# Performance work log

Hardware: AMD Instinct MI355X
Metric: run time of the kernel (lower is better)

The kernel has to match this reference:

```python
import jax, jax.numpy as jnp
import numpy as np

TAU = 2.0   # spikingjelly LIFNode default tau
VTH = 1.0   # config.vthreshold

@jax.custom_vjp
def atan_spike(x):
    # heaviside forward, ATan surrogate backward (spikingjelly surrogate.ATan, alpha=2)
    return (x >= 0).astype(x.dtype)

def _atan_fwd(x):
    return atan_spike(x), x

def _atan_bwd(x, g):
    alpha = 2.0
    return (g * (alpha / 2.0) / (1.0 + (jnp.pi / 2.0 * alpha * x) ** 2),)

atan_spike.defvjp(_atan_fwd, _atan_bwd)

def layer_norm(x, eps=1e-6):
    m = jnp.mean(x, axis=-1, keepdims=True)
    v = jnp.mean((x - m) ** 2, axis=-1, keepdims=True)
    return (x - m) * jax.lax.rsqrt(v + eps)

def time_shift(x):
    # ZeroPad2d((0,0,1,-1)): xx[:, t] = x[:, t-1], xx[:, 0] = 0
    return jnp.pad(x, ((0, 0), (1, 0), (0, 0)))[:, :-1]

def lif_multistep(x4):
    # spikingjelly LIFNode, step_mode='m', decay_input=True, hard reset to v_reset=0
    def step(v, xt):
        v = v + (xt - v) / TAU
        s = atan_spike(v - VTH)
        return v * (1.0 - s), s
    _, spikes = jax.lax.scan(step, jnp.zeros_like(x4[0]), x4)
    return spikes

def wkv(w, u, k, v):
    # RWKV-v4 numerically-stable WKV scan. w: [C] (negative), u: [C], k,v: [B,T,C]
    B, T, C = k.shape
    def step(carry, kv):
        aa, bb, pp = carry
        kt, vt = kv
        ww = u + kt
        p = jnp.maximum(pp, ww)
        e1 = jnp.exp(pp - p); e2 = jnp.exp(ww - p)
        y = (e1 * aa + e2 * vt) / (e1 * bb + e2)
        ww2 = pp + w
        p2 = jnp.maximum(ww2, kt)
        f1 = jnp.exp(ww2 - p2); f2 = jnp.exp(kt - p2)
        return (f1 * aa + f2 * vt, f1 * bb + f2, p2), y
    init = (jnp.zeros((B, C), k.dtype), jnp.zeros((B, C), k.dtype),
            jnp.full((B, C), -1e38, k.dtype))
    _, ys = jax.lax.scan(step, init, (jnp.moveaxis(k, 1, 0), jnp.moveaxis(v, 1, 0)))
    return jnp.moveaxis(ys, 0, 1)

def time_mix(h, time_decay, time_first, tmk, tmv, tmr, Wk, Wv, Wr, Wo):
    xx = time_shift(h)
    xk = h * tmk + xx * (1 - tmk)
    xv = h * tmv + xx * (1 - tmv)
    xr = h * tmr + xx * (1 - tmr)
    k = jnp.einsum('btc,oc->bto', xk, Wk)
    v = jnp.einsum('btc,oc->bto', xv, Wv)
    sr = jax.nn.sigmoid(jnp.einsum('btc,oc->bto', xr, Wr))
    y = wkv(-jnp.exp(time_decay), time_first, k, v)
    return jnp.einsum('btc,oc->bto', sr * y, Wo)

def channel_mix(h, cmk, cmr, Wck, Wcv, Wcr):
    xx = time_shift(h)
    xk = h * cmk + xx * (1 - cmk)
    xr = h * cmr + xx * (1 - cmr)
    k = jnp.square(jax.nn.relu(jnp.einsum('btc,hc->bth', xk, Wck)))
    kv = jnp.einsum('bth,ch->btc', k, Wcv)
    return jax.nn.sigmoid(jnp.einsum('btc,oc->bto', xr, Wcr)) * kv

def _forward(x, rt, time_decay, time_first, tmix_k, tmix_v, tmix_r,
             Wk, Wv, Wr, Wo, cmix_k, cmix_r, Wck, Wcv, Wcr,
             Wrm, brm, Wam, bam):
    B, P1, C = x.shape
    xc = jnp.concatenate([x, jnp.broadcast_to(rt, (B, P1, C))], axis=1)  # [B, 2*P1, C]
    att = time_mix(layer_norm(xc), time_decay, time_first,
                   tmix_k, tmix_v, tmix_r, Wk, Wv, Wr, Wo)
    att = lif_multistep(jnp.broadcast_to(att, (4,) + att.shape)).mean(0)
    xc = xc + att
    ffn = channel_mix(layer_norm(xc), cmix_k, cmix_r, Wck, Wcv, Wcr)
    ffn = lif_multistep(jnp.broadcast_to(ffn, (4,) + ffn.shape)).mean(0)
    xc = xc + ffn
    xo, rtok = xc[:, :P1], xc[:, P1:]
    r = jnp.einsum('bpc,qc->bpq', rtok, Wrm) + brm   # restruction_token_MLP [B,P1,P1]
    r = jnp.swapaxes(r, 1, 2)                        # permute(0,2,1)
    r = jnp.einsum('bpq,cq->bpc', r, Wam) + bam      # another_MLP [B,P1,C]
    return xo + xo * r

def setup_inputs() -> dict:
    key = jax.random.key(0)
    ks = jax.random.split(key, 20)
    B, P1, C = 8, 256, 1024
    H = 4 * C
    s = 0.02
    f32 = jnp.float32
    return {
        'x': jax.random.normal(ks[0], (B, P1, C), f32),
        'rt': jax.random.normal(ks[1], (1, P1, C), f32) * 0.5,
        'time_decay': jax.random.normal(ks[2], (C,), f32),
        'time_first': jax.random.normal(ks[3], (C,), f32) * 0.3,
        'tmix_k': jax.random.uniform(ks[4], (1, 1, C), f32),
        'tmix_v': jax.random.uniform(ks[5], (1, 1, C), f32),
        'tmix_r': jax.random.uniform(ks[6], (1, 1, C), f32),
        'Wk': jax.random.normal(ks[7], (C, C), f32) * s,
        'Wv': jax.random.normal(ks[8], (C, C), f32) * s,
        'Wr': jax.random.normal(ks[9], (C, C), f32) * s,
        'Wo': jax.random.normal(ks[10], (C, C), f32) * s,
        'cmix_k': jax.random.uniform(ks[11], (1, 1, C), f32),
        'cmix_r': jax.random.uniform(ks[12], (1, 1, C), f32),
        'Wck': jax.random.normal(ks[13], (H, C), f32) * s,
        'Wcv': jax.random.normal(ks[14], (C, H), f32) * s,
        'Wcr': jax.random.normal(ks[15], (C, C), f32) * s,
        'Wrm': jax.random.normal(ks[16], (P1, C), f32) * s,
        'brm': jax.random.normal(ks[17], (P1,), f32) * s,
        'Wam': jax.random.normal(ks[18], (C, P1), f32) * s,
        'bam': jax.random.normal(ks[19], (C,), f32) * s,
    }

def reference(x, rt, time_decay, time_first, tmix_k, tmix_v, tmix_r,
              Wk, Wv, Wr, Wo, cmix_k, cmix_r, Wck, Wcv, Wcr,
              Wrm, brm, Wam, bam):
    return _forward(x, rt, time_decay, time_first, tmix_k, tmix_v, tmix_r,
                    Wk, Wv, Wr, Wo, cmix_k, cmix_r, Wck, Wcv, Wcr,
                    Wrm, brm, Wam, bam)
```

## Files before the change

kernel.cpp:

```cpp
#include <hip/hip_runtime.h>
#include <hip/hip_bf16.h>
#include <math.h>
#include <stdint.h>

#define TB_ 8
#define TT_ 512
#define TC_ 1024
#define WKV_NCH 32
#define WKV_L 16

typedef __attribute__((ext_vector_type(8))) short bf16x8;
typedef __attribute__((ext_vector_type(4))) short s16x4;
typedef __attribute__((ext_vector_type(4))) float f32x4;

__device__ __forceinline__ float b2f(short u) {
  union { unsigned int i; float f; } x;
  x.i = ((unsigned int)(unsigned short)u) << 16;
  return x.f;
}
__device__ __forceinline__ short f2b(float f) {
  __hip_bfloat16 h = __float2bfloat16(f);
  return __builtin_bit_cast(short, h);
}
__device__ __forceinline__ float sigm(float x) { return 1.0f / (1.0f + expf(-x)); }

__device__ __forceinline__ float lif4(float a) {
  float v = 0.0f, acc = 0.0f;
#pragma unroll
  for (int i = 0; i < 4; ++i) {
    v += (a - v) * 0.5f;
    float s = (v >= 1.0f) ? 1.0f : 0.0f;
    acc += s;
    v *= (1.0f - s);
  }
  return acc * 0.25f;
}

__device__ __forceinline__ void gload16(const void* g, void* l) {
  __builtin_amdgcn_global_load_lds(
      (__attribute__((address_space(1))) void*)(g),
      (__attribute__((address_space(3))) void*)(l), 16, 0, 0);
}

template <int N>
__device__ __forceinline__ void waitv() {
  if constexpr (N == 0)  asm volatile("s_waitcnt vmcnt(0)" ::: "memory");
  else if constexpr (N == 2)  asm volatile("s_waitcnt vmcnt(2)" ::: "memory");
  else if constexpr (N == 4)  asm volatile("s_waitcnt vmcnt(4)" ::: "memory");
  else if constexpr (N == 8)  asm volatile("s_waitcnt vmcnt(8)" ::: "memory");
  else if constexpr (N == 12) asm volatile("s_waitcnt vmcnt(12)" ::: "memory");
  else static_assert(N == 0, "unsupported vmcnt");
}
__device__ __forceinline__ void barrier_() {
  asm volatile("s_barrier" ::: "memory");
}


__global__ __launch_bounds__(256) void ln_mix3(
    const float* __restrict__ x, const float* __restrict__ rt,
    const float* __restrict__ tmk, const float* __restrict__ tmv,
    const float* __restrict__ tmr, float* __restrict__ xc,
    short* __restrict__ xk, short* __restrict__ xv, short* __restrict__ xr) {
  __shared__ float red[256];
  int row = blockIdx.x;
  int t = row & 511, b = row >> 9;
  int tid = threadIdx.x;
  const float* src = (t < 256) ? x + (int64_t)(b * 256 + t) * TC_
                               : rt + (int64_t)(t - 256) * TC_;
  float4 v = ((const float4*)src)[tid];
  ((float4*)(xc + (int64_t)row * TC_))[tid] = v;
  red[tid] = v.x + v.y + v.z + v.w;
  __syncthreads();
  for (int off = 128; off > 0; off >>= 1) {
    if (tid < off) red[tid] += red[tid + off];
    __syncthreads();
  }
  float mean = red[0] * (1.0f / 1024.0f);
  __syncthreads();
  float dx = v.x - mean, dy = v.y - mean, dz = v.z - mean, dw = v.w - mean;
  red[tid] = dx * dx + dy * dy + dz * dz + dw * dw;
  __syncthreads();
  for (int off = 128; off > 0; off >>= 1) {
    if (tid < off) red[tid] += red[tid + off];
    __syncthreads();
  }
  float rs = 1.0f / sqrtf(red[0] * (1.0f / 1024.0f) + 1e-6f);
  float c0 = dx * rs, c1 = dy * rs, c2 = dz * rs, c3 = dw * rs;
  float p0 = 0.f, p1 = 0.f, p2 = 0.f, p3 = 0.f;
  if (t > 0) {
    int tp = t - 1;
    const float* srcp = (tp < 256) ? x + (int64_t)(b * 256 + tp) * TC_
                                   : rt + (int64_t)(tp - 256) * TC_;
    __syncthreads();
    float4 w4 = ((const float4*)srcp)[tid];
    red[tid] = w4.x + w4.y + w4.z + w4.w;
    __syncthreads();
    for (int off = 128; off > 0; off >>= 1) {
      if (tid < off) red[tid] += red[tid + off];
      __syncthreads();
    }
    float meanp = red[0] * (1.0f / 1024.0f);
    __syncthreads();
    float ex = w4.x - meanp, ey = w4.y - meanp, ez = w4.z - meanp,
          ew = w4.w - meanp;
    red[tid] = ex * ex + ey * ey + ez * ez + ew * ew;
    __syncthreads();
    for (int off = 128; off > 0; off >>= 1) {
      if (tid < off) red[tid] += red[tid + off];
      __syncthreads();
    }
    float rsp = 1.0f / sqrtf(red[0] * (1.0f / 1024.0f) + 1e-6f);
    p0 = ex * rsp; p1 = ey * rsp; p2 = ez * rsp; p3 = ew * rsp;
  }
  int c = tid * 4;
  int64_t o = (int64_t)row * TC_ + c;
  float m0, m1, m2, m3;
  s16x4 ov;
  m0 = tmk[c]; m1 = tmk[c + 1]; m2 = tmk[c + 2]; m3 = tmk[c + 3];
  ov.x = f2b(c0 * m0 + p0 * (1.0f - m0));
  ov.y = f2b(c1 * m1 + p1 * (1.0f - m1));
  ov.z = f2b(c2 * m2 + p2 * (1.0f - m2));
  ov.w = f2b(c3 * m3 + p3 * (1.0f - m3));
  *(s16x4*)(xk + o) = ov;
  m0 = tmv[c]; m1 = tmv[c + 1]; m2 = tmv[c + 2]; m3 = tmv[c + 3];
  ov.x = f2b(c0 * m0 + p0 * (1.0f - m0));
  ov.y = f2b(c1 * m1 + p1 * (1.0f - m1));
  ov.z = f2b(c2 * m2 + p2 * (1.0f - m2));
  ov.w = f2b(c3 * m3 + p3 * (1.0f - m3));
  *(s16x4*)(xv + o) = ov;
  m0 = tmr[c]; m1 = tmr[c + 1]; m2 = tmr[c + 2]; m3 = tmr[c + 3];
  ov.x = f2b(c0 * m0 + p0 * (1.0f - m0));
  ov.y = f2b(c1 * m1 + p1 * (1.0f - m1));
  ov.z = f2b(c2 * m2 + p2 * (1.0f - m2));
  ov.w = f2b(c3 * m3 + p3 * (1.0f - m3));
  *(s16x4*)(xr + o) = ov;
}

__global__ __launch_bounds__(256) void ln_mix2(const float* __restrict__ xc,
                                               const float* __restrict__ cmk,
                                               const float* __restrict__ cmr,
                                               short* __restrict__ xk,
                                               short* __restrict__ xr) {
  __shared__ float red[256];
  int row = blockIdx.x;
  int t = row & 511;
  int tid = threadIdx.x;
  float4 v = ((const float4*)(xc + (int64_t)row * TC_))[tid];
  red[tid] = v.x + v.y + v.z + v.w;
  __syncthreads();
  for (int off = 128; off > 0; off >>= 1) {
    if (tid < off) red[tid] += red[tid + off];
    __syncthreads();
  }
  float mean = red[0] * (1.0f / 1024.0f);
  __syncthreads();
  float dx = v.x - mean, dy = v.y - mean, dz = v.z - mean, dw = v.w - mean;
  red[tid] = dx * dx + dy * dy + dz * dz + dw * dw;
  __syncthreads();
  for (int off = 128; off > 0; off >>= 1) {
    if (tid < off) red[tid] += red[tid + off];
    __syncthreads();
  }
  float rs = 1.0f / sqrtf(red[0] * (1.0f / 1024.0f) + 1e-6f);
  float c0 = dx * rs, c1 = dy * rs, c2 = dz * rs, c3 = dw * rs;
  float p0 = 0.f, p1 = 0.f, p2 = 0.f, p3 = 0.f;
  if (t > 0) {
    __syncthreads();
    float4 w4 = ((const float4*)(xc + (int64_t)(row - 1) * TC_))[tid];
    red[tid] = w4.x + w4.y + w4.z + w4.w;
    __syncthreads();
    for (int off = 128; off > 0; off >>= 1) {
      if (tid < off) red[tid] += red[tid + off];
      __syncthreads();
    }
    float meanp = red[0] * (1.0f / 1024.0f);
    __syncthreads();
    float ex = w4.x - meanp, ey = w4.y - meanp, ez = w4.z - meanp,
          ew = w4.w - meanp;
    red[tid] = ex * ex + ey * ey + ez * ez + ew * ew;
    __syncthreads();
    for (int off = 128; off > 0; off >>= 1) {
      if (tid < off) red[tid] += red[tid + off];
      __syncthreads();
    }
    float rsp = 1.0f / sqrtf(red[0] * (1.0f / 1024.0f) + 1e-6f);
    p0 = ex * rsp; p1 = ey * rsp; p2 = ez * rsp; p3 = ew * rsp;
  }
  int c = tid * 4;
  float k0 = cmk[c], k1 = cmk[c + 1], k2 = cmk[c + 2], k3 = cmk[c + 3];
  float r0 = cmr[c], r1 = cmr[c + 1], r2 = cmr[c + 2], r3 = cmr[c + 3];
  s16x4 ok, orr;
  ok.x = f2b(c0 * k0 + p0 * (1.0f - k0));
  ok.y = f2b(c1 * k1 + p1 * (1.0f - k1));
  ok.z = f2b(c2 * k2 + p2 * (1.0f - k2));
  ok.w = f2b(c3 * k3 + p3 * (1.0f - k3));
  orr.x = f2b(c0 * r0 + p0 * (1.0f - r0));
  orr.y = f2b(c1 * r1 + p1 * (1.0f - r1));
  orr.z = f2b(c2 * r2 + p2 * (1.0f - r2));
  orr.w = f2b(c3 * r3 + p3 * (1.0f - r3));
  *(s16x4*)(xk + (int64_t)row * TC_ + c) = ok;
  *(s16x4*)(xr + (int64_t)row * TC_ + c) = orr;
}

__global__ __launch_bounds__(256) void cvt_b(const float* __restrict__ src,
                                             short* __restrict__ dst) {
  int64_t i = (int64_t)(blockIdx.x * 256 + threadIdx.x) * 8;
  float4 a = *(const float4*)(src + i);
  float4 b = *(const float4*)(src + i + 4);
  bf16x8 o;
  o[0] = f2b(a.x); o[1] = f2b(a.y); o[2] = f2b(a.z); o[3] = f2b(a.w);
  o[4] = f2b(b.x); o[5] = f2b(b.y); o[6] = f2b(b.z); o[7] = f2b(b.w);
  *(bf16x8*)(dst + i) = o;
}

__global__ __launch_bounds__(256) void cvt_rtok(const float* __restrict__ xc,
                                                short* __restrict__ dst) {
  int i = blockIdx.x * 256 + threadIdx.x;
  int b = i >> 15;
  int rem = i & 32767;
  const float* s = xc + (int64_t)b * 524288 + 262144 + (int64_t)rem * 8;
  float4 a = *(const float4*)s;
  float4 c = *(const float4*)(s + 4);
  bf16x8 o;
  o[0] = f2b(a.x); o[1] = f2b(a.y); o[2] = f2b(a.z); o[3] = f2b(a.w);
  o[4] = f2b(c.x); o[5] = f2b(c.y); o[6] = f2b(c.z); o[7] = f2b(c.w);
  *(bf16x8*)(dst + (int64_t)i * 8) = o;
}

__global__ __launch_bounds__(256) void cvt_all(
    const float* __restrict__ Wk, const float* __restrict__ Wv,
    const float* __restrict__ Wr, const float* __restrict__ Wo,
    const float* __restrict__ Wcr, const float* __restrict__ Wcv,
    const float* __restrict__ Wrm, const float* __restrict__ Wam,
    short* __restrict__ bWk, short* __restrict__ bWv, short* __restrict__ bWr,
    short* __restrict__ bWo, short* __restrict__ bWcr, short* __restrict__ bWcv,
    short* __restrict__ bWrm, short* __restrict__ bWam,
    float* __restrict__ S) {
  int bid = blockIdx.x;
  if (bid >= 4864) {
    int row = (bid - 4864) * 4 + (threadIdx.x >> 6);
    int lane = threadIdx.x & 63;
    float4 v = ((const float4*)(Wam + (int64_t)row * 256))[lane];
    float s = v.x + v.y + v.z + v.w;
    for (int off = 32; off > 0; off >>= 1) s += __shfl_down(s, off);
    if (lane == 0) S[row] = s;
    return;
  }
  const float* src; short* dst; int base;
  if (bid < 512)       { src = Wk;  dst = bWk;  base = bid; }
  else if (bid < 1024) { src = Wv;  dst = bWv;  base = bid - 512; }
  else if (bid < 1536) { src = Wr;  dst = bWr;  base = bid - 1024; }
  else if (bid < 2048) { src = Wo;  dst = bWo;  base = bid - 1536; }
  else if (bid < 2560) { src = Wcr; dst = bWcr; base = bid - 2048; }
  else if (bid < 4608) { src = Wcv; dst = bWcv; base = bid - 2560; }
  else if (bid < 4736) { src = Wrm; dst = bWrm; base = bid - 4608; }
  else                 { src = Wam; dst = bWam; base = bid - 4736; }
  int64_t i = ((int64_t)base * 256 + threadIdx.x) * 8;
  float4 a = *(const float4*)(src + i);
  float4 b = *(const float4*)(src + i + 4);
  bf16x8 o;
  o[0] = f2b(a.x); o[1] = f2b(a.y); o[2] = f2b(a.z); o[3] = f2b(a.w);
  o[4] = f2b(b.x); o[5] = f2b(b.y); o[6] = f2b(b.z); o[7] = f2b(b.w);
  *(bf16x8*)(dst + i) = o;
}

__global__ __launch_bounds__(256) void wkv_p1(const float* __restrict__ td,
                                              const short* __restrict__ K,
                                              const short* __restrict__ V,
                                              float* __restrict__ Ca,
                                              float* __restrict__ Da,
                                              float* __restrict__ Qa) {
  int bx = blockIdx.x;
  int ch = bx >> 5;
  int b = (bx >> 2) & 7;
  int c = (bx & 3) * 256 + threadIdx.x;
  float w = -expf(td[c]);
  float aa = 0.0f, bb = 0.0f, pp = -1e38f;
  int64_t base = ((int64_t)b * TT_ + ch * WKV_L) * TC_ + c;
#pragma unroll
  for (int t = 0; t < WKV_L; ++t) {
    int64_t o = base + (int64_t)t * TC_;
    float kt = b2f(K[o]), vt = b2f(V[o]);
    float ww2 = pp + w;
    float p2 = fmaxf(ww2, kt);
    float e1 = expf(ww2 - p2);
    float e2 = expf(kt - p2);
    aa = e1 * aa + e2 * vt;
    bb = e1 * bb + e2;
    pp = p2;
  }
  int idx = ch * 8192 + b * 1024 + c;
  Ca[idx] = aa; Da[idx] = bb; Qa[idx] = pp;
}

__global__ __launch_bounds__(256) void wkv_p2(const float* __restrict__ td,
                                              const float* __restrict__ Ca,
                                              const float* __restrict__ Da,
                                              const float* __restrict__ Qa,
                                              float* __restrict__ Aa,
                                              float* __restrict__ Ba,
                                              float* __restrict__ Pa) {
  int i = blockIdx.x * 256 + threadIdx.x;
  int c = i & (TC_ - 1);
  float wL = -expf(td[c]) * (float)WKV_L;
  float aa = 0.0f, bb = 0.0f, pp = -1e38f;
#pragma unroll 4
  for (int ch = 0; ch < WKV_NCH; ++ch) {
    int idx = ch * 8192 + i;
    Aa[idx] = aa; Ba[idx] = bb; Pa[idx] = pp;
    float ppw = pp + wL;
    float q = Qa[idx];
    float p2 = fmaxf(ppw, q);
    float ea = expf(ppw - p2);
    float eb = expf(q - p2);
    aa = aa * ea + Ca[idx] * eb;
    bb = bb * ea + Da[idx] * eb;
    pp = p2;
  }
}

__global__ __launch_bounds__(256) void wkv_p3(const float* __restrict__ td,
                                              const float* __restrict__ tf,
                                              const short* __restrict__ K,
                                              const short* __restrict__ V,
                                              const short* __restrict__ SR,
                                              short* __restrict__ SRY,
                                              const float* __restrict__ Aa,
                                              const float* __restrict__ Ba,
                                              const float* __restrict__ Pa) {
  int bx = blockIdx.x;
  int ch = bx >> 5;
  int b = (bx >> 2) & 7;
  int c = (bx & 3) * 256 + threadIdx.x;
  float w = -expf(td[c]);
  float u = tf[c];
  int idx = ch * 8192 + b * 1024 + c;
  float aa = Aa[idx], bb = Ba[idx], pp = Pa[idx];
  int64_t base = ((int64_t)b * TT_ + ch * WKV_L) * TC_ + c;
#pragma unroll
  for (int t = 0; t < WKV_L; ++t) {
    int64_t o = base + (int64_t)t * TC_;
    float kt = b2f(K[o]), vt = b2f(V[o]);
    float ww = u + kt;
    float p = fmaxf(pp, ww);
    float E1 = expf(pp - p);
    float E2 = expf(ww - p);
    float y = (E1 * aa + E2 * vt) / (E1 * bb + E2);
    SRY[o] = f2b(y * b2f(SR[o]));
    float ww2 = pp + w;
    float p2 = fmaxf(ww2, kt);
    float e1 = expf(ww2 - p2);
    float e2 = expf(kt - p2);
    aa = e1 * aa + e2 * vt;
    bb = e1 * bb + e2;
    pp = p2;
  }
}

template <int EPI>
__global__ __launch_bounds__(512, 1) void gemm2p(
    const short* __restrict__ A, const short* __restrict__ B,
    void* __restrict__ Cp, int M, int N, int K, int Kst,
    const float* __restrict__ e0, const float* __restrict__ e1,
    const float* __restrict__ e2, const void* __restrict__ e3) {
  __shared__ short lds[2 * 32768];
  const int tid = threadIdx.x;

  const unsigned gx = gridDim.x, gy = gridDim.y;
  const unsigned nwg = gx * gy;
  const unsigned lin = blockIdx.x + gx * blockIdx.y;
  const unsigned cs = nwg >> 3;
  const unsigned nl = (lin & 7) * cs + (lin >> 3);
  const unsigned bxs = nl % gx;
  const unsigned bys = nl / gx;

  const int brow = bys * 128;
  const int bcol = bxs * 128;

  const int srow = ((tid >> 6) << 4) + (tid & 15);
  const int skc = ((tid >> 4) & 3) * 8;
  const short* gA = A + (int64_t)(brow + srow) * Kst + skc;
  const short* gB = B + (int64_t)(bcol + srow) * Kst + skc;

  const int lane = tid & 63, wid = tid >> 6;
  const int wr = wid >> 2, wc = wid & 3;

  f32x4 acc[4][2] = {};

#define RD_A(rb, kh, m) \
  (*(const bf16x8*)(lds + (rb) * 32768 + (kh) * 8192 + (wr * 4 + (m)) * 512 + lane * 8))
#define RD_B(rb, kh, n) \
  (*(const bf16x8*)(lds + (rb) * 32768 + 16384 + (kh) * 8192 + (wc * 2 + (n)) * 512 + lane * 8))
#define ST_A(sb, kh, kt) \
  gload16(gA + (kt) * 64 + (kh) * 32, lds + (sb) * 32768 + (kh) * 8192 + tid * 8)
#define ST_B(sb, kh, kt) \
  gload16(gB + (kt) * 64 + (kh) * 32, lds + (sb) * 32768 + 16384 + (kh) * 8192 + tid * 8)
#define MM(am, bn, i, j) \
  acc[i][j] = __builtin_amdgcn_mfma_f32_16x16x32_bf16(am, bn, acc[i][j], 0, 0, 0)

  const int nt = K / 64;
  ST_A(0, 0, 0); ST_B(0, 0, 0); ST_A(0, 1, 0); ST_B(0, 1, 0);
  waitv<2>();
  barrier_();

  for (int t = 0; t < nt - 1; ++t) {
    const int rb = t & 1, sb = rb ^ 1, kn = t + 1;
    {
      bf16x8 a0 = RD_A(rb, 0, 0), a1 = RD_A(rb, 0, 1);
      bf16x8 a2 = RD_A(rb, 0, 2), a3 = RD_A(rb, 0, 3);
      bf16x8 b0 = RD_B(rb, 0, 0), b1 = RD_B(rb, 0, 1);
      ST_A(sb, 0, kn); ST_B(sb, 0, kn);
      MM(a0, b0, 0, 0); MM(a0, b1, 0, 1); MM(a1, b0, 1, 0); MM(a1, b1, 1, 1);
      MM(a2, b0, 2, 0); MM(a2, b1, 2, 1); MM(a3, b0, 3, 0); MM(a3, b1, 3, 1);
      waitv<2>();
      barrier_();
    }
    {
      bf16x8 a0 = RD_A(rb, 1, 0), a1 = RD_A(rb, 1, 1);
      bf16x8 a2 = RD_A(rb, 1, 2), a3 = RD_A(rb, 1, 3);
      bf16x8 b0 = RD_B(rb, 1, 0), b1 = RD_B(rb, 1, 1);
      ST_A(sb, 1, kn); ST_B(sb, 1, kn);
      MM(a0, b0, 0, 0); MM(a0, b1, 0, 1); MM(a1, b0, 1, 0); MM(a1, b1, 1, 1);
      MM(a2, b0, 2, 0); MM(a2, b1, 2, 1); MM(a3, b0, 3, 0); MM(a3, b1, 3, 1);
      waitv<2>();
      barrier_();
    }
  }
  {
    waitv<0>();
    barrier_();
    const int rb = (nt - 1) & 1;
#pragma unroll
    for (int kh = 0; kh < 2; ++kh) {
      bf16x8 a0 = RD_A(rb, kh, 0), a1 = RD_A(rb, kh, 1);
      bf16x8 a2 = RD_A(rb, kh, 2), a3 = RD_A(rb, kh, 3);
      bf16x8 b0 = RD_B(rb, kh, 0), b1 = RD_B(rb, kh, 1);
      MM(a0, b0, 0, 0); MM(a0, b1, 0, 1); MM(a1, b0, 1, 0); MM(a1, b1, 1, 1);
      MM(a2, b0, 2, 0); MM(a2, b1, 2, 1); MM(a3, b0, 3, 0); MM(a3, b1, 3, 1);
    }
  }
#undef RD_A
#undef RD_B
#undef ST_A
#undef ST_B
#undef MM

  const int r0 = brow + wr * 64 + (lane >> 4) * 4;
  const int c0 = bcol + wc * 32 + (lane & 15);
#pragma unroll
  for (int m = 0; m < 4; ++m) {
#pragma unroll
    for (int j = 0; j < 4; ++j) {
      int row = r0 + m * 16 + j;
#pragma unroll
      for (int n = 0; n < 2; ++n) {
        int col = c0 + n * 16;
        float v = acc[m][n][j];
        int64_t idx = (int64_t)row * N + col;
        if (EPI == 1) {
          ((short*)Cp)[idx] = f2b(sigm(v));
        } else if (EPI == 4) {
          float* XC = (float*)Cp;
          XC[idx] = XC[idx] + lif4(v);
        } else if (EPI == 5) {
          float* XC = (float*)Cp;
          float srr = b2f(((const short*)e3)[idx]);
          XC[idx] = XC[idx] + lif4(v * srr);
        }
      }
    }
  }
}

template <int EPI>
__global__ __launch_bounds__(512, 1) void gemm256(
    const short* __restrict__ A, const short* __restrict__ B,
    void* __restrict__ Cp, int M, int N, int K, int Kst,
    int64_t sA, int64_t sB, int64_t sC) {
  __shared__ short lds[2 * 32768];
  const int tid = threadIdx.x;

  const unsigned gx = gridDim.x, gy = gridDim.y;
  const unsigned nwg = gx * gy * gridDim.z;
  const unsigned lin = blockIdx.x + gx * (blockIdx.y + gy * blockIdx.z);
  const unsigned cs = nwg >> 3;
  const unsigned nl = (lin & 7) * cs + (lin >> 3);
  const unsigned bxs = nl % gx;
  const unsigned tmp = nl / gx;
  const unsigned bys = tmp % gy;
  const unsigned bz = tmp / gy;

  const int brow = bys * 256;
  const int bcol = bxs * 256;
  const short* Ab = A + bz * sA;
  const short* Bb = B + bz * sB;

  const short* gA[2];
  const short* gB[2];
  int loff[2];
#pragma unroll
  for (int c = 0; c < 2; ++c) {
    int p = c * 512 + tid;
    int u = p >> 6, s = p & 63;
    gA[c] = Ab + (int64_t)(brow + u * 16 + (s & 15)) * Kst + (s >> 4) * 8;
    gB[c] = Bb + (int64_t)(bcol + u * 16 + (s & 15)) * Kst + (s >> 4) * 8;
    loff[c] = p * 8;
  }

  const int lane = tid & 63, wid = tid >> 6;
  const int wr = wid >> 2, wc = wid & 3;

  f32x4 acc[8][4] = {};

#define RD_A(rb, kh, m) \
  (*(const bf16x8*)(lds + (rb) * 32768 + (kh) * 8192 + (wr * 8 + (m)) * 512 + lane * 8))
#define RD_B(rb, kh, n) \
  (*(const bf16x8*)(lds + (rb) * 32768 + 16384 + (kh) * 8192 + (wc * 4 + (n)) * 512 + lane * 8))
#define ST_A(sb, kh, kt)                                                     \
  {                                                                          \
    gload16(gA[0] + (kt) * 64 + (kh) * 32,                                   \
            lds + (sb) * 32768 + (kh) * 8192 + loff[0]);                     \
    gload16(gA[1] + (kt) * 64 + (kh) * 32,                                   \
            lds + (sb) * 32768 + (kh) * 8192 + loff[1]);                     \
  }
#define ST_B(sb, kh, kt)                                                     \
  {                                                                          \
    gload16(gB[0] + (kt) * 64 + (kh) * 32,                                   \
            lds + (sb) * 32768 + 16384 + (kh) * 8192 + loff[0]);             \
    gload16(gB[1] + (kt) * 64 + (kh) * 32,                                   \
            lds + (sb) * 32768 + 16384 + (kh) * 8192 + loff[1]);             \
  }
#define MM(am, bn, i, j) \
  acc[i][j] = __builtin_amdgcn_mfma_f32_16x16x32_bf16(am, bn, acc[i][j], 0, 0, 0)

  const int nt = K / 64;
  ST_A(0, 0, 0); ST_B(0, 0, 0); ST_A(0, 1, 0); ST_B(0, 1, 0);
  waitv<4>();
  barrier_();

  for (int t = 0; t < nt - 1; ++t) {
    const int rb = t & 1, sb = rb ^ 1, kn = t + 1;
    bf16x8 b0, b1, b2, b3;
    {
      bf16x8 a0 = RD_A(rb, 0, 0), a1 = RD_A(rb, 0, 1);
      bf16x8 a2 = RD_A(rb, 0, 2), a3 = RD_A(rb, 0, 3);
      b0 = RD_B(rb, 0, 0); b1 = RD_B(rb, 0, 1);
      b2 = RD_B(rb, 0, 2); b3 = RD_B(rb, 0, 3);
      ST_A(sb, 0, kn);
      MM(a0, b0, 0, 0); MM(a0, b1, 0, 1); MM(a0, b2, 0, 2); MM(a0, b3, 0, 3);
      MM(a1, b0, 1, 0); MM(a1, b1, 1, 1); MM(a1, b2, 1, 2); MM(a1, b3, 1, 3);
      MM(a2, b0, 2, 0); MM(a2, b1, 2, 1); MM(a2, b2, 2, 2); MM(a2, b3, 2, 3);
      MM(a3, b0, 3, 0); MM(a3, b1, 3, 1); MM(a3, b2, 3, 2); MM(a3, b3, 3, 3);
      barrier_();
    }
    {
      bf16x8 a4 = RD_A(rb, 0, 4), a5 = RD_A(rb, 0, 5);
      bf16x8 a6 = RD_A(rb, 0, 6), a7 = RD_A(rb, 0, 7);
      ST_B(sb, 0, kn);
      MM(a4, b0, 4, 0); MM(a4, b1, 4, 1); MM(a4, b2, 4, 2); MM(a4, b3, 4, 3);
      MM(a5, b0, 5, 0); MM(a5, b1, 5, 1); MM(a5, b2, 5, 2); MM(a5, b3, 5, 3);
      MM(a6, b0, 6, 0); MM(a6, b1, 6, 1); MM(a6, b2, 6, 2); MM(a6, b3, 6, 3);
      MM(a7, b0, 7, 0); MM(a7, b1, 7, 1); MM(a7, b2, 7, 2); MM(a7, b3, 7, 3);
      waitv<4>();
      barrier_();
    }
    {
      bf16x8 a0 = RD_A(rb, 1, 0), a1 = RD_A(rb, 1, 1);
      bf16x8 a2 = RD_A(rb, 1, 2), a3 = RD_A(rb, 1, 3);
      b0 = RD_B(rb, 1, 0); b1 = RD_B(rb, 1, 1);
      b2 = RD_B(rb, 1, 2); b3 = RD_B(rb, 1, 3);
      ST_A(sb, 1, kn);
      MM(a0, b0, 0, 0); MM(a0, b1, 0, 1); MM(a0, b2, 0, 2); MM(a0, b3, 0, 3);
      MM(a1, b0, 1, 0); MM(a1, b1, 1, 1); MM(a1, b2, 1, 2); MM(a1, b3, 1, 3);
      MM(a2, b0, 2, 0); MM(a2, b1, 2, 1); MM(a2, b2, 2, 2); MM(a2, b3, 2, 3);
      MM(a3, b0, 3, 0); MM(a3, b1, 3, 1); MM(a3, b2, 3, 2); MM(a3, b3, 3, 3);
      barrier_();
    }
    {
      bf16x8 a4 = RD_A(rb, 1, 4), a5 = RD_A(rb, 1, 5);
      bf16x8 a6 = RD_A(rb, 1, 6), a7 = RD_A(rb, 1, 7);
      ST_B(sb, 1, kn);
      MM(a4, b0, 4, 0); MM(a4, b1, 4, 1); MM(a4, b2, 4, 2); MM(a4, b3, 4, 3);
      MM(a5, b0, 5, 0); MM(a5, b1, 5, 1); MM(a5, b2, 5, 2); MM(a5, b3, 5, 3);
      MM(a6, b0, 6, 0); MM(a6, b1, 6, 1); MM(a6, b2, 6, 2); MM(a6, b3, 6, 3);
      MM(a7, b0, 7, 0); MM(a7, b1, 7, 1); MM(a7, b2, 7, 2); MM(a7, b3, 7, 3);
      waitv<4>();
      barrier_();
    }
  }
  {
    waitv<0>();
    barrier_();
    const int rb = (nt - 1) & 1;
#pragma unroll
    for (int kh = 0; kh < 2; ++kh) {
      bf16x8 b0 = RD_B(rb, kh, 0), b1 = RD_B(rb, kh, 1);
      bf16x8 b2 = RD_B(rb, kh, 2), b3 = RD_B(rb, kh, 3);
#pragma unroll
      for (int m = 0; m < 8; ++m) {
        bf16x8 am = RD_A(rb, kh, m);
        MM(am, b0, m, 0); MM(am, b1, m, 1);
        MM(am, b2, m, 2); MM(am, b3, m, 3);
      }
    }
  }
#undef RD_A
#undef RD_B
#undef ST_A
#undef ST_B
#undef MM

  const int r0 = brow + wr * 128 + (lane >> 4) * 4;
  const int c0 = bcol + wc * 64 + (lane & 15);
#pragma unroll
  for (int m = 0; m < 8; ++m) {
#pragma unroll
    for (int j = 0; j < 4; ++j) {
      int row = r0 + m * 16 + j;
#pragma unroll
      for (int n = 0; n < 4; ++n) {
        int col = c0 + n * 16;
        float v = acc[m][n][j];
        int64_t idx = bz * sC + (int64_t)row * N + col;
        if (EPI == 2) {
          v = fmaxf(v, 0.0f);
          ((short*)Cp)[idx] = f2b(v * v);
        } else if (EPI == 6) {
          ((short*)Cp)[idx] = f2b(bz == 2 ? sigm(v) : v);
        }
      }
    }
  }
}

template <int BM, int BN, int EPI, int D, int MINW>
__global__ __launch_bounds__(256, MINW) void gemm_bf16(
    const short* __restrict__ A, const short* __restrict__ B,
    void* __restrict__ Cp, int M, int N, int K, int Kst,
    int64_t sA, int64_t sB, int64_t sC,
    const float* __restrict__ e0, const float* __restrict__ e1,
    const float* __restrict__ e2, const void* __restrict__ e3, int64_t sE) {
  constexpr int MF = BM / 32;
  constexpr int NF = BN / 32;
  constexpr int ASLOT = BM / 64;
  constexpr int BSLOT = BN / 64;
  constexpr int NL = ASLOT + BSLOT;
  constexpr int SBUF = (BM + BN) * 32;
  __shared__ short lds[D * SBUF];
  const int tid = threadIdx.x;

  const unsigned gx = gridDim.x, gy = gridDim.y;
  const unsigned nwg = gx * gy * gridDim.z;
  const unsigned lin = blockIdx.x + gx * (blockIdx.y + gy * blockIdx.z);
  const unsigned cs = nwg >> 3;
  const unsigned nl = (lin & 7) * cs + (lin >> 3);
  const unsigned bxs = nl % gx;
  const unsigned tmp = nl / gx;
  const unsigned bys = tmp % gy;
  const unsigned bz = tmp / gy;

  const int brow = bys * BM;
  const int bcol = bxs * BN;
  const short* Ab = A + bz * sA;
  const short* Bb = B + bz * sB;

  const int srow = ((tid >> 6) << 4) + (tid & 15);
  const int skc = ((tid >> 4) & 3) * 8;
  const short* gA[ASLOT];
  const short* gB[BSLOT];
#pragma unroll
  for (int s = 0; s < ASLOT; ++s)
    gA[s] = Ab + (int64_t)(brow + s * 64 + srow) * Kst + skc;
#pragma unroll
  for (int s = 0; s < BSLOT; ++s)
    gB[s] = Bb + (int64_t)(bcol + s * 64 + srow) * Kst + skc;

  const int lane = tid & 63, wid = tid >> 6;
  const int wr = wid >> 1, wc = wid & 1;

  f32x4 acc[MF][NF] = {};

  auto stage = [&](int buf, int k0) {
    short* d = lds + buf * SBUF;
#pragma unroll
    for (int s = 0; s < ASLOT; ++s)
      gload16(gA[s] + k0, d + s * 2048 + tid * 8);
#pragma unroll
    for (int s = 0; s < BSLOT; ++s)
      gload16(gB[s] + k0, d + BM * 32 + s * 2048 + tid * 8);
  };
  auto compute = [&](int buf) {
    const short* base = lds + buf * SBUF;
    bf16x8 af[MF], bfv[NF];
#pragma unroll
    for (int m = 0; m < MF; ++m)
      af[m] = *(const bf16x8*)(base + (wr * MF + m) * 512 + lane * 8);
#pragma unroll
    for (int n = 0; n < NF; ++n)
      bfv[n] = *(const bf16x8*)(base + BM * 32 + (wc * NF + n) * 512 + lane * 8);
#pragma unroll
    for (int m = 0; m < MF; ++m)
#pragma unroll
      for (int n = 0; n < NF; ++n)
        acc[m][n] = __builtin_amdgcn_mfma_f32_16x16x32_bf16(af[m], bfv[n],
                                                            acc[m][n], 0, 0, 0);
  };

  const int nst = K / 32;
#pragma unroll
  for (int d = 0; d < D - 1; ++d) stage(d, d * 32);
  for (int t = 0; t <= nst - D; ++t) {
    stage((t + D - 1) & (D - 1), (t + D - 1) * 32);
    waitv<(D - 1) * NL>();
    barrier_();
    compute(t & (D - 1));
    barrier_();
  }
  {
    int t = nst - D + 1;
    if constexpr (D >= 4) {
      waitv<2 * NL>(); barrier_(); compute(t & (D - 1)); barrier_(); ++t;
      waitv<1 * NL>(); barrier_(); compute(t & (D - 1)); barrier_(); ++t;
    }
    waitv<0>(); barrier_(); compute(t & (D - 1));
  }

  const int r0 = brow + wr * (BM / 2) + (lane >> 4) * 4;
  const int c0 = bcol + wc * (BN / 2) + (lane & 15);
#pragma unroll
  for (int m = 0; m < MF; ++m) {
#pragma unroll
    for (int j = 0; j < 4; ++j) {
      int row = r0 + m * 16 + j;
#pragma unroll
      for (int n = 0; n < NF; ++n) {
        int col = c0 + n * 16;
        float v = acc[m][n][j];
        int64_t idx = (int64_t)row * N + col;
        if (EPI == 0) {
          ((short*)Cp)[bz * sC + idx] = f2b(v);
        } else if (EPI == 3) {
          float r2 = v + e0[row] * e1[col] + e2[col];
          float xo = ((const float*)e3)[bz * sE + idx];
          ((float*)Cp)[bz * sC + idx] = xo * (1.0f + r2);
        }
      }
    }
  }
}

extern "C" void kernel_launch(void* const* d_in, const int* in_sizes, int n_in,
                              void* d_out, int out_size, void* d_ws,
                              size_t ws_size, hipStream_t stream) {
  const float* x   = (const float*)d_in[0];
  const float* rt  = (const float*)d_in[1];
  const float* td  = (const float*)d_in[2];
  const float* tf  = (const float*)d_in[3];
  const float* tmk = (const float*)d_in[4];
  const float* tmv = (const float*)d_in[5];
  const float* tmr = (const float*)d_in[6];
  const float* Wk  = (const float*)d_in[7];
  const float* Wv  = (const float*)d_in[8];
  const float* Wr  = (const float*)d_in[9];
  const float* Wo  = (const float*)d_in[10];
  const float* cmk = (const float*)d_in[11];
  const float* cmr = (const float*)d_in[12];
  const float* Wck = (const float*)d_in[13];
  const float* Wcv = (const float*)d_in[14];
  const float* Wcr = (const float*)d_in[15];
  const float* Wrm = (const float*)d_in[16];
  const float* brm = (const float*)d_in[17];
  const float* Wam = (const float*)d_in[18];
  const float* bam = (const float*)d_in[19];
  float* out = (float*)d_out;

  const size_t MB = 1ull << 20;
  uint8_t* W8 = (uint8_t*)d_ws;
  float* XC   = (float*)(W8);
  short* S1   = (short*)(W8 + 24 * MB);
  short* S2   = (short*)(W8 + 32 * MB);
  short* S3   = (short*)(W8 + 40 * MB);
  short* bWcv = (short*)(W8 + 48 * MB);
  short* bWk  = (short*)(W8 + 56 * MB);
  short* bWo  = (short*)(W8 + 62 * MB);
  short* bWcr = (short*)(W8 + 64 * MB);
  short* bWrm = (short*)(W8 + 66 * MB);
  short* bWam = (short*)(W8 + 66 * MB + 512 * 1024);
  short* KK   = (short*)(W8 + 67 * MB);
  short* VV   = (short*)(W8 + 75 * MB);
  short* RR   = (short*)(W8 + 83 * MB);
  float* Ca   = (float*)(W8 + 91 * MB);
  float* Da   = (float*)(W8 + 92 * MB);
  float* Qa   = (float*)(W8 + 93 * MB);
  float* Aa   = (float*)(W8 + 94 * MB);
  float* Ba   = (float*)(W8 + 95 * MB);
  float* Pa   = (float*)(W8 + 96 * MB);
  short* SRY  = S1;
  short* xk2  = S2;
  short* xr2  = S3;
  short* SRR  = S1;
  short* bWck = S3;
  short* H16  = KK;
  short* rtok = S2;
  short* Mt   = (short*)(W8 + 36 * MB);
  float* Sb   = (float*)(W8 + 99 * MB);

  dim3 blk(256);
  dim3 blk512(512);

  cvt_all<<<5120, blk, 0, stream>>>(Wk, Wv, Wr, Wo, Wcr, Wcv, Wrm, Wam,
                                    bWk, bWk + 1048576, bWk + 2097152, bWo,
                                    bWcr, bWcv, bWrm, bWam, Sb);

  ln_mix3<<<TB_ * TT_, blk, 0, stream>>>(x, rt, tmk, tmv, tmr, XC, S1, S2, S3);

  gemm256<6><<<dim3(4, 16, 3), blk512, 0, stream>>>(
      S1, bWk, KK, 4096, 1024, 1024, 1024, 4194304, 1048576, 4194304);
  wkv_p1<<<WKV_NCH * TB_ * 4, blk, 0, stream>>>(td, KK, VV, Ca, Da, Qa);
  wkv_p2<<<32, blk, 0, stream>>>(td, Ca, Da, Qa, Aa, Ba, Pa);
  wkv_p3<<<WKV_NCH * TB_ * 4, blk, 0, stream>>>(td, tf, KK, VV, RR, SRY,
                                                Aa, Ba, Pa);
  gemm2p<4><<<dim3(8, 32), blk512, 0, stream>>>(
      SRY, bWo, XC, 4096, 1024, 1024, 1024, nullptr, nullptr, nullptr,
      nullptr);
  ln_mix2<<<TB_ * TT_, blk, 0, stream>>>(XC, cmk, cmr, xk2, xr2);
  gemm2p<1><<<dim3(8, 32), blk512, 0, stream>>>(
      xr2, bWcr, SRR, 4096, 1024, 1024, 1024, nullptr, nullptr, nullptr,
      nullptr);
  cvt_b<<<2048, blk, 0, stream>>>(Wck, bWck);
  gemm256<2><<<dim3(16, 16), blk512, 0, stream>>>(
      xk2, bWck, H16, 4096, 4096, 1024, 1024, 0, 0, 0);
  gemm2p<5><<<dim3(8, 32), blk512, 0, stream>>>(
      H16, bWcv, XC, 4096, 1024, 4096, 4096, nullptr, nullptr, nullptr, SRR);
  cvt_rtok<<<1024, blk, 0, stream>>>(XC, rtok);
  gemm_bf16<64, 64, 0, 2, 2><<<dim3(4, 4, 8), blk, 0, stream>>>(
      bWrm, rtok, Mt, 256, 256, 1024, 1024, 0, (int64_t)256 * 1024,
      (int64_t)256 * 256, nullptr, nullptr, nullptr, nullptr, 0);
  gemm_bf16<64, 64, 3, 2, 2><<<dim3(16, 4, 8), blk, 0, stream>>>(
      Mt, bWam, out, 256, 1024, 256, 256, (int64_t)256 * 256, 0,
      (int64_t)256 * 1024, brm, Sb, bam, XC, (int64_t)512 * 1024);
}
```

Measured before the change: 299.9 us.

## Merge Wck conversion into cvt_all and fuse channel-mix GEMMs into one launch

The separate cvt_b launch that converted Wck to bf16 is removed, and that work is folded into cvt_all through extra blocks, using a new dedicated workspace buffer. The sigmoid-receptance GEMM (xr2·Wcr) and the squared-ReLU key GEMM (xk2·Wck) now run in a single 320-block gemm256_hs launch that shares a common 256x256 tile body, with the epilogue chosen at runtime. This is meant to cut launch count and fill the GPU better, since the 64 tiles of the smaller GEMM run alongside the 256 tiles of the larger one. The cost is a runtime epilogue branch instead of a compile-time template, and unused vmcnt paths and the gemm2p template parameters are also removed.

```diff
diff --git a/kernel.cpp b/kernel.cpp
--- a/kernel.cpp
+++ b/kernel.cpp
@@ -47,8 +47,6 @@
   if constexpr (N == 0)  asm volatile("s_waitcnt vmcnt(0)" ::: "memory");
   else if constexpr (N == 2)  asm volatile("s_waitcnt vmcnt(2)" ::: "memory");
   else if constexpr (N == 4)  asm volatile("s_waitcnt vmcnt(4)" ::: "memory");
-  else if constexpr (N == 8)  asm volatile("s_waitcnt vmcnt(8)" ::: "memory");
-  else if constexpr (N == 12) asm volatile("s_waitcnt vmcnt(12)" ::: "memory");
   else static_assert(N == 0, "unsupported vmcnt");
 }
 __device__ __forceinline__ void barrier_() {
@@ -202,17 +200,6 @@
   *(s16x4*)(xr + (int64_t)row * TC_ + c) = orr;
 }
 
-__global__ __launch_bounds__(256) void cvt_b(const float* __restrict__ src,
-                                             short* __restrict__ dst) {
-  int64_t i = (int64_t)(blockIdx.x * 256 + threadIdx.x) * 8;
-  float4 a = *(const float4*)(src + i);
-  float4 b = *(const float4*)(src + i + 4);
-  bf16x8 o;
-  o[0] = f2b(a.x); o[1] = f2b(a.y); o[2] = f2b(a.z); o[3] = f2b(a.w);
-  o[4] = f2b(b.x); o[5] = f2b(b.y); o[6] = f2b(b.z); o[7] = f2b(b.w);
-  *(bf16x8*)(dst + i) = o;
-}
-
 __global__ __launch_bounds__(256) void cvt_rtok(const float* __restrict__ xc,
                                                 short* __restrict__ dst) {
   int i = blockIdx.x * 256 + threadIdx.x;
@@ -232,12 +219,13 @@
     const float* __restrict__ Wr, const float* __restrict__ Wo,
     const float* __restrict__ Wcr, const float* __restrict__ Wcv,
     const float* __restrict__ Wrm, const float* __restrict__ Wam,
+    const float* __restrict__ Wck,
     short* __restrict__ bWk, short* __restrict__ bWv, short* __restrict__ bWr,
     short* __restrict__ bWo, short* __restrict__ bWcr, short* __restrict__ bWcv,
     short* __restrict__ bWrm, short* __restrict__ bWam,
-    float* __restrict__ S) {
+    short* __restrict__ bWck, float* __restrict__ S) {
   int bid = blockIdx.x;
-  if (bid >= 4864) {
+  if (bid >= 4864 && bid < 5120) {
     int row = (bid - 4864) * 4 + (threadIdx.x >> 6);
     int lane = threadIdx.x & 63;
     float4 v = ((const float4*)(Wam + (int64_t)row * 256))[lane];
@@ -254,7 +242,8 @@
   else if (bid < 2560) { src = Wcr; dst = bWcr; base = bid - 2048; }
   else if (bid < 4608) { src = Wcv; dst = bWcv; base = bid - 2560; }
   else if (bid < 4736) { src = Wrm; dst = bWrm; base = bid - 4608; }
-  else                 { src = Wam; dst = bWam; base = bid - 4736; }
+  else if (bid < 4864) { src = Wam; dst = bWam; base = bid - 4736; }
+  else                 { src = Wck; dst = bWck; base = bid - 5120; }
   int64_t i = ((int64_t)base * 256 + threadIdx.x) * 8;
   float4 a = *(const float4*)(src + i);
   float4 b = *(const float4*)(src + i + 4);
@@ -361,8 +350,7 @@
 __global__ __launch_bounds__(512, 1) void gemm2p(
     const short* __restrict__ A, const short* __restrict__ B,
     void* __restrict__ Cp, int M, int N, int K, int Kst,
-    const float* __restrict__ e0, const float* __restrict__ e1,
-    const float* __restrict__ e2, const void* __restrict__ e3) {
+    const void* __restrict__ e3) {
   __shared__ short lds[2 * 32768];
   const int tid = threadIdx.x;
 
@@ -457,9 +445,7 @@
         int col = c0 + n * 16;
         float v = acc[m][n][j];
         int64_t idx = (int64_t)row * N + col;
-        if (EPI == 1) {
-          ((short*)Cp)[idx] = f2b(sigm(v));
-        } else if (EPI == 4) {
+        if (EPI == 4) {
           float* XC = (float*)Cp;
           XC[idx] = XC[idx] + lif4(v);
         } else if (EPI == 5) {
@@ -472,29 +458,11 @@
   }
 }
 
-template <int EPI>
-__global__ __launch_bounds__(512, 1) void gemm256(
-    const short* __restrict__ A, const short* __restrict__ B,
-    void* __restrict__ Cp, int M, int N, int K, int Kst,
-    int64_t sA, int64_t sB, int64_t sC) {
-  __shared__ short lds[2 * 32768];
+__device__ __forceinline__ void g256_body(
+    short* lds, const short* __restrict__ A, const short* __restrict__ B,
+    short* __restrict__ Cp, int N, int K, int Kst, int brow, int bcol,
+    int epi) {
   const int tid = threadIdx.x;
-
-  const unsigned gx = gridDim.x, gy = gridDim.y;
-  const unsigned nwg = gx * gy * gridDim.z;
-  const unsigned lin = blockIdx.x + gx * (blockIdx.y + gy * blockIdx.z);
-  const unsigned cs = nwg >> 3;
-  const unsigned nl = (lin & 7) * cs + (lin >> 3);
-  const unsigned bxs = nl % gx;
-  const unsigned tmp = nl / gx;
-  const unsigned bys = tmp % gy;
-  const unsigned bz = tmp / gy;
-
-  const int brow = bys * 256;
-  const int bcol = bxs * 256;
-  const short* Ab = A + bz * sA;
-  const short* Bb = B + bz * sB;
-
   const short* gA[2];
   const short* gB[2];
   int loff[2];
@@ -502,8 +470,8 @@
   for (int c = 0; c < 2; ++c) {
     int p = c * 512 + tid;
     int u = p >> 6, s = p & 63;
-    gA[c] = Ab + (int64_t)(brow + u * 16 + (s & 15)) * Kst + (s >> 4) * 8;
-    gB[c] = Bb + (int64_t)(bcol + u * 16 + (s & 15)) * Kst + (s >> 4) * 8;
+    gA[c] = A + (int64_t)(brow + u * 16 + (s & 15)) * Kst + (s >> 4) * 8;
+    gB[c] = B + (int64_t)(bcol + u * 16 + (s & 15)) * Kst + (s >> 4) * 8;
     loff[c] = p * 8;
   }
 
@@ -621,15 +589,47 @@
       for (int n = 0; n < 4; ++n) {
         int col = c0 + n * 16;
         float v = acc[m][n][j];
-        int64_t idx = bz * sC + (int64_t)row * N + col;
-        if (EPI == 2) {
-          v = fmaxf(v, 0.0f);
-          ((short*)Cp)[idx] = f2b(v * v);
-        } else if (EPI == 6) {
-          ((short*)Cp)[idx] = f2b(bz == 2 ? sigm(v) : v);
-        }
+        if (epi == 1) v = sigm(v);
+        else if (epi == 2) { v = fmaxf(v, 0.0f); v = v * v; }
+        Cp[(int64_t)row * N + col] = f2b(v);
       }
     }
+  }
+}
+
+__global__ __launch_bounds__(512, 1) void gemm256_z(
+    const short* __restrict__ A, const short* __restrict__ B,
+    short* __restrict__ C, int64_t sA, int64_t sB, int64_t sC) {
+  __shared__ short lds[2 * 32768];
+  const unsigned gx = gridDim.x, gy = gridDim.y;
+  const unsigned nwg = gx * gy * gridDim.z;
+  const unsigned lin = blockIdx.x + gx * (blockIdx.y + gy * blockIdx.z);
+  const unsigned cs = nwg >> 3;
+  const unsigned nl = (lin & 7) * cs + (lin >> 3);
+  const unsigned bxs = nl % gx;
+  const unsigned tmp = nl / gx;
+  const unsigned bys = tmp % gy;
+  const unsigned bz = tmp / gy;
+  g256_body(lds, A + bz * sA, B + bz * sB, C + bz * sC, 1024, 1024, 1024,
+            bys * 256, bxs * 256, bz == 2 ? 1 : 0);
+}
+
+__global__ __launch_bounds__(512, 1) void gemm256_hs(
+    const short* __restrict__ xk2, const short* __restrict__ bWck,
+    short* __restrict__ H16, const short* __restrict__ xr2,
+    const short* __restrict__ bWcr, short* __restrict__ SRR) {
+  __shared__ short lds[2 * 32768];
+  const unsigned nwg = gridDim.x;
+  const unsigned lin = blockIdx.x;
+  const unsigned cs = nwg >> 3;
+  const unsigned nl = (lin & 7) * cs + (lin >> 3);
+  if (nl < 256) {
+    g256_body(lds, xk2, bWck, H16, 4096, 1024, 1024, (nl >> 4) * 256,
+              (nl & 15) * 256, 2);
+  } else {
+    unsigned r = nl - 256;
+    g256_body(lds, xr2, bWcr, SRR, 1024, 1024, 1024, (r >> 2) * 256,
+              (r & 3) * 256, 1);
   }
 }
 
@@ -718,10 +718,6 @@
   }
   {
     int t = nst - D + 1;
-    if constexpr (D >= 4) {
-      waitv<2 * NL>(); barrier_(); compute(t & (D - 1)); barrier_(); ++t;
-      waitv<1 * NL>(); barrier_(); compute(t & (D - 1)); barrier_(); ++t;
-    }
     waitv<0>(); barrier_(); compute(t & (D - 1));
   }
 
@@ -776,62 +772,56 @@
 
   const size_t MB = 1ull << 20;
   uint8_t* W8 = (uint8_t*)d_ws;
-  float* XC   = (float*)(W8);
-  short* S1   = (short*)(W8 + 24 * MB);
-  short* S2   = (short*)(W8 + 32 * MB);
-  short* S3   = (short*)(W8 + 40 * MB);
-  short* bWcv = (short*)(W8 + 48 * MB);
-  short* bWk  = (short*)(W8 + 56 * MB);
-  short* bWo  = (short*)(W8 + 62 * MB);
-  short* bWcr = (short*)(W8 + 64 * MB);
-  short* bWrm = (short*)(W8 + 66 * MB);
-  short* bWam = (short*)(W8 + 66 * MB + 512 * 1024);
-  short* KK   = (short*)(W8 + 67 * MB);
-  short* VV   = (short*)(W8 + 75 * MB);
-  short* RR   = (short*)(W8 + 83 * MB);
-  float* Ca   = (float*)(W8 + 91 * MB);
-  float* Da   = (float*)(W8 + 92 * MB);
-  float* Qa   = (float*)(W8 + 93 * MB);
-  float* Aa   = (float*)(W8 + 94 * MB);
-  float* Ba   = (float*)(W8 + 95 * MB);
-  float* Pa   = (float*)(W8 + 96 * MB);
-  short* SRY  = S1;
-  short* xk2  = S2;
-  short* xr2  = S3;
-  short* SRR  = S1;
-  short* bWck = S3;
-  short* H16  = KK;
-  short* rtok = S2;
-  short* Mt   = (short*)(W8 + 36 * MB);
-  float* Sb   = (float*)(W8 + 99 * MB);
+  float* XC    = (float*)(W8);
+  short* bWck16 = (short*)(W8 + 16 * MB);
+  short* S1    = (short*)(W8 + 24 * MB);
+  short* S2    = (short*)(W8 + 32 * MB);
+  short* S3    = (short*)(W8 + 40 * MB);
+  short* bWcv  = (short*)(W8 + 48 * MB);
+  short* bWk   = (short*)(W8 + 56 * MB);
+  short* bWo   = (short*)(W8 + 62 * MB);
+  short* bWcr  = (short*)(W8 + 64 * MB);
+  short* bWrm  = (short*)(W8 + 66 * MB);
+  short* bWam  = (short*)(W8 + 66 * MB + 512 * 1024);
+  short* KK    = (short*)(W8 + 67 * MB);
+  short* VV    = (short*)(W8 + 75 * MB);
+  short* RR    = (short*)(W8 + 83 * MB);
+  float* Ca    = (float*)(W8 + 91 * MB);
+  float* Da    = (float*)(W8 + 92 * MB);
+  float* Qa    = (float*)(W8 + 93 * MB);
+  float* Aa    = (float*)(W8 + 94 * MB);
+  float* Ba    = (float*)(W8 + 95 * MB);
+  float* Pa    = (float*)(W8 + 96 * MB);
+  short* SRY   = S1;
+  short* xk2   = S2;
+  short* xr2   = S3;
+  short* SRR   = S1;
+  short* H16   = KK;
+  short* rtok  = S2;
+  short* Mt    = (short*)(W8 + 36 * MB);
+  float* Sb    = (float*)(W8 + 99 * MB);
 
   dim3 blk(256);
   dim3 blk512(512);
 
-  cvt_all<<<5120, blk, 0, stream>>>(Wk, Wv, Wr, Wo, Wcr, Wcv, Wrm, Wam,
+  cvt_all<<<7168, blk, 0, stream>>>(Wk, Wv, Wr, Wo, Wcr, Wcv, Wrm, Wam, Wck,
                                     bWk, bWk + 1048576, bWk + 2097152, bWo,
-                                    bWcr, bWcv, bWrm, bWam, Sb);
+                                    bWcr, bWcv, bWrm, bWam, bWck16, Sb);
 
   ln_mix3<<<TB_ * TT_, blk, 0, stream>>>(x, rt, tmk, tmv, tmr, XC, S1, S2, S3);
 
-  gemm256<6><<<dim3(4, 16, 3), blk512, 0, stream>>>(
-      S1, bWk, KK, 4096, 1024, 1024, 1024, 4194304, 1048576, 4194304);
+  gemm256_z<<<dim3(4, 16, 3), blk512, 0, stream>>>(
+      S1, bWk, KK, 4194304, 1048576, 4194304);
   wkv_p1<<<WKV_NCH * TB_ * 4, blk, 0, stream>>>(td, KK, VV, Ca, Da, Qa);
   wkv_p2<<<32, blk, 0, stream>>>(td, Ca, Da, Qa, Aa, Ba, Pa);
   wkv_p3<<<WKV_NCH * TB_ * 4, blk, 0, stream>>>(td, tf, KK, VV, RR, SRY,
                                                 Aa, Ba, Pa);
   gemm2p<4><<<dim3(8, 32), blk512, 0, stream>>>(
-      SRY, bWo, XC, 4096, 1024, 1024, 1024, nullptr, nullptr, nullptr,
-      nullptr);
+      SRY, bWo, XC, 4096, 1024, 1024, 1024, nullptr);
   ln_mix2<<<TB_ * TT_, blk, 0, stream>>>(XC, cmk, cmr, xk2, xr2);
-  gemm2p<1><<<dim3(8, 32), blk512, 0, stream>>>(
-      xr2, bWcr, SRR, 4096, 1024, 1024, 1024, nullptr, nullptr, nullptr,
-      nullptr);
-  cvt_b<<<2048, blk, 0, stream>>>(Wck, bWck);
-  gemm256<2><<<dim3(16, 16), blk512, 0, stream>>>(
-      xk2, bWck, H16, 4096, 4096, 1024, 1024, 0, 0, 0);
+  gemm256_hs<<<320, blk512, 0, stream>>>(xk2, bWck16, H16, xr2, bWcr, SRR);
   gemm2p<5><<<dim3(8, 32), blk512, 0, stream>>>(
-      H16, bWcv, XC, 4096, 1024, 4096, 4096, nullptr, nullptr, nullptr, SRR);
+      H16, bWcv, XC, 4096, 1024, 4096, 4096, SRR);
   cvt_rtok<<<1024, blk, 0, stream>>>(XC, rtok);
   gemm_bf16<64, 64, 0, 2, 2><<<dim3(4, 4, 8), blk, 0, stream>>>(
       bWrm, rtok, Mt, 256, 256, 1024, 1024, 0, (int64_t)256 * 1024,
```

After: 322.0 us. +7.4%, slower.
